# Kernel optimization log

Measured on AMD Instinct MI355X. Metric: run time of the kernel, lower is better.

The kernel has to match this reference:

```python
import jax, jax.numpy as jnp
import numpy as np

B, N, E = 2, 2048, 1024
H = 16
D = E // H  # head_dim = 64
MLP = 4096
EPS = 1e-5


def _layernorm(x, g, b):
    mu = jnp.mean(x, axis=-1, keepdims=True)
    var = jnp.var(x, axis=-1, keepdims=True)
    return (x - mu) * jax.lax.rsqrt(var + EPS) * g + b


def setup_inputs() -> dict:
    key = jax.random.key(0)
    ks = jax.random.split(key, 12)
    s_e = 1.0 / np.sqrt(E)
    s_m = 1.0 / np.sqrt(MLP)
    return {
        "x": jax.random.normal(ks[0], (B, N, E), jnp.float32),
        "w_qkv": jax.random.uniform(ks[1], (E, 3 * E), jnp.float32, -s_e, s_e),
        "b_qkv": jax.random.uniform(ks[2], (3 * E,), jnp.float32, -s_e, s_e),
        "w_proj": jax.random.uniform(ks[3], (E, E), jnp.float32, -s_e, s_e),
        "b_proj": jax.random.uniform(ks[4], (E,), jnp.float32, -s_e, s_e),
        "g1": jnp.ones((E,), jnp.float32),
        "beta1": jnp.zeros((E,), jnp.float32),
        "g2": jnp.ones((E,), jnp.float32),
        "beta2": jnp.zeros((E,), jnp.float32),
        "w_fc1": jax.random.uniform(ks[5], (E, MLP), jnp.float32, -s_e, s_e),
        "b_fc1": jax.random.uniform(ks[6], (MLP,), jnp.float32, -s_e, s_e),
        "w_fc2": jax.random.uniform(ks[7], (MLP, E), jnp.float32, -s_m, s_m),
        "b_fc2": jax.random.uniform(ks[8], (E,), jnp.float32, -s_m, s_m),
    }


def reference(x, w_qkv, b_qkv, w_proj, b_proj, g1, beta1, g2, beta2,
              w_fc1, b_fc1, w_fc2, b_fc2):
    scale = D ** (-0.5)
    # --- attention block (pre-norm) ---
    h = _layernorm(x, g1, beta1)
    qkv = (h @ w_qkv + b_qkv).reshape(B, N, 3, H, D)
    q, k, v = (qkv[:, :, i].transpose(0, 2, 1, 3) for i in range(3))  # [B,H,N,D]
    scores = jnp.einsum("bhnd,bhmd->bhnm", q, k) * scale  # [B,H,N,N]
    attn = jax.nn.softmax(scores, axis=-1)
    out = jnp.einsum("bhnm,bhmd->bhnd", attn, v)
    out = out.transpose(0, 2, 1, 3).reshape(B, N, E)
    x = x + (out @ w_proj + b_proj)
    # --- MLP block (pre-norm, exact GELU as in torch default) ---
    h = _layernorm(x, g2, beta2)
    h = jax.nn.gelu(h @ w_fc1 + b_fc1, approximate=False) @ w_fc2 + b_fc2
    return x + h
```

## Files before the change

kernel.cpp:

```cpp
#include <hip/hip_runtime.h>
#include <hip/hip_bf16.h>
#include <cmath>


typedef __hip_bfloat16 bf16;
typedef __bf16 bf16x8 __attribute__((ext_vector_type(8)));
typedef __bf16 bf16x4v __attribute__((ext_vector_type(4)));
typedef float  f32x4  __attribute__((ext_vector_type(4)));

#define CB 2
#define CN 2048
#define CE 1024
#define CH 16
#define CD 64
#define CMLP 4096
#define CM (CB*CN)

#define PS 136

#if __has_builtin(__builtin_amdgcn_exp2f)
#define EXP2F __builtin_amdgcn_exp2f
#else
#define EXP2F exp2f
#endif
#define SM_SCALE_LOG2E 0.18033688011112042f

__device__ __forceinline__ float b2f(bf16 v){ return __bfloat162float(v); }
__device__ __forceinline__ bf16  f2b(float v){ return __float2bfloat16(v); }

__device__ __forceinline__ void gl_lds16(const void* g, void* l){
  __builtin_amdgcn_global_load_lds((__attribute__((address_space(1))) void*)g,
                                   (__attribute__((address_space(3))) void*)l,
                                   16, 0, 0);
}

__global__ __launch_bounds__(256) void transpose_k(const float* __restrict__ in,
                                                   bf16* __restrict__ out,
                                                   int K, int N){
  __shared__ float tile[32][33];
  const int n0 = blockIdx.x*32, k0 = blockIdx.y*32;
  const int tx = threadIdx.x & 31;
  const int ty = threadIdx.x >> 5;
  #pragma unroll
  for(int i=0;i<32;i+=8) tile[ty+i][tx] = in[(size_t)(k0+ty+i)*N + n0+tx];
  __syncthreads();
  #pragma unroll
  for(int i=0;i<32;i+=8) out[(size_t)(n0+ty+i)*K + k0+tx] = f2b(tile[tx][ty+i]);
}

__global__ __launch_bounds__(256) void ln_k(const float* __restrict__ x,
                                            const float* __restrict__ g,
                                            const float* __restrict__ be,
                                            bf16* __restrict__ out){
  const int row = blockIdx.x;
  const int t = threadIdx.x;
  const float4 v4 = ((const float4*)(x + (size_t)row*CE))[t];
  float v[4] = {v4.x, v4.y, v4.z, v4.w};
  float s=0.f, s2=0.f;
  #pragma unroll
  for(int i=0;i<4;i++){ s+=v[i]; s2+=v[i]*v[i]; }
  #pragma unroll
  for(int off=32; off>0; off>>=1){ s += __shfl_down(s,off); s2 += __shfl_down(s2,off); }
  __shared__ float red[8];
  __shared__ float mu_s, rs_s;
  const int wv=t>>6, ln=t&63;
  if(ln==0){ red[wv]=s; red[4+wv]=s2; }
  __syncthreads();
  if(t==0){
    float S=red[0]+red[1]+red[2]+red[3], S2=red[4]+red[5]+red[6]+red[7];
    float mu=S/CE;
    mu_s=mu; rs_s=rsqrtf(S2/CE - mu*mu + 1e-5f);
  }
  __syncthreads();
  const float mu=mu_s, rs=rs_s;
  #pragma unroll
  for(int i=0;i<4;i++){
    int c=t*4+i;
    out[(size_t)row*CE+c] = f2b((v[i]-mu)*rs*g[c] + be[c]);
  }
}

#define EP_QKV 0
#define EP_GELU 2

template<int MODE>
__global__ __launch_bounds__(512,2) void gemm256_k(
  const bf16* __restrict__ A, const bf16* __restrict__ BT,
  const float* __restrict__ bias,
  bf16* __restrict__ Cb, bf16* __restrict__ Cq, bf16* __restrict__ Ck,
  bf16* __restrict__ Cv, int Ksz, int Nsz)
{
  __shared__ __align__(16) bf16 Alds[2][256*64];
  __shared__ __align__(16) bf16 Blds[2][256*64];
  const int tid = threadIdx.x;
  const int wave = tid>>6, lane = tid&63;
  const int m16 = lane&15, quad = lane>>4;
  const int sw = m16&7;
  const int wi = wave>>2, wj = wave&3;

  const int lin = blockIdx.x + gridDim.x*blockIdx.y;
  const int m_idx = (lin&7) + 8*((lin>>3)&1);
  const int n_idx = lin>>4;
  const size_t m0 = (size_t)m_idx*256;
  const size_t n0 = (size_t)n_idx*256;

  f32x4 acc[8][4] = {};

  const int srow8 = lane>>3;
  const int schk  = ((lane&7)^srow8)*8;
  const bf16* pA = A  + (m0 + 32*wave + srow8)*(size_t)Ksz + schk;
  const bf16* pB = BT + (n0 + 32*wave + srow8)*(size_t)Ksz + schk;

  auto stage = [&](int buf, const bf16* gA, const bf16* gB){
    bf16* lA = &Alds[buf][wave*2048];
    bf16* lB = &Blds[buf][wave*2048];
    #pragma unroll
    for(int j=0;j<4;j++) gl_lds16(gA + (size_t)(j*8)*Ksz, lA + j*512);
    #pragma unroll
    for(int j=0;j<4;j++) gl_lds16(gB + (size_t)(j*8)*Ksz, lB + j*512);
  };
  auto compute = [&](int buf){
    #pragma unroll
    for(int w=0;w<2;w++){
      bf16x8 af[8], bfr[4];
      #pragma unroll
      for(int i=0;i<8;i++){
        const int row = wi*128+16*i+m16;
        af[i] = *(const bf16x8*)(&Alds[buf][row*64 + ((w*4+quad)^sw)*8]);
      }
      #pragma unroll
      for(int j=0;j<4;j++){
        const int row = wj*64+16*j+m16;
        bfr[j] = *(const bf16x8*)(&Blds[buf][row*64 + ((w*4+quad)^sw)*8]);
      }
      #pragma unroll
      for(int i=0;i<8;i++)
        #pragma unroll
        for(int j=0;j<4;j++)
          acc[i][j] = __builtin_amdgcn_mfma_f32_16x16x32_bf16(af[i], bfr[j], acc[i][j], 0,0,0);
    }
  };

  const int kIters = Ksz/64;
  stage(0, pA, pB); pA += 64; pB += 64;
  for(int kb=0; kb<kIters; ++kb){
    __syncthreads();
    if(kb+1<kIters){ stage((kb+1)&1, pA, pB); pA += 64; pB += 64; }
    compute(kb&1);
  }

  #pragma unroll
  for(int i=0;i<8;i++){
    #pragma unroll
    for(int j=0;j<4;j++){
      const int col = (int)n0 + wj*64 + 16*j + m16;
      const float bcol = bias[col];
      #pragma unroll
      for(int r=0;r<4;r++){
        const int row = (int)m0 + wi*128 + 16*i + quad*4 + r;
        float v = acc[i][j][r] + bcol;
        if constexpr (MODE==EP_QKV){
          const int b = row>>11, n = row&2047;
          const int which = col>>10, cc = col&1023;
          const int h = cc>>6, d = cc&63;
          if(which==0)      Cq[(((size_t)(b*CH+h))*CN+n)*CD + d] = f2b(v);
          else if(which==1) Ck[(((size_t)(b*CH+h))*CN+n)*CD + d] = f2b(v);
          else              Cv[(((size_t)(b*CH+h))*CD+d)*CN + n] = f2b(v);
        } else {
          const float u2 = 1.5957691216f*(v + 0.044715f*v*v*v);
          v = v * (1.f/(1.f + __expf(-u2)));
          Cb[(size_t)row*Nsz+col] = f2b(v);
        }
      }
    }
  }
}

__global__ __launch_bounds__(512,2) void gemm128_k(
  const bf16* __restrict__ A, const bf16* __restrict__ BT,
  const float* __restrict__ bias, const float* __restrict__ res,
  float* __restrict__ Cf, int Ksz, int Nsz)
{
  __shared__ __align__(16) bf16 Alds[2][128*128];
  __shared__ __align__(16) bf16 Blds[2][128*128];
  const int tid = threadIdx.x;
  const int wave = tid>>6, lane = tid&63;
  const int m16 = lane&15, quad = lane>>4;
  const int sw = m16&7;
  const int wi = wave>>2, wj = wave&3;

  const int lin = blockIdx.x + gridDim.x*blockIdx.y;
  const int m_idx = (lin&7) + 8*((lin>>3)&3);
  const int n_idx = lin>>5;
  const size_t m0 = (size_t)m_idx*128;
  const size_t n0 = (size_t)n_idx*128;

  f32x4 acc[4][2] = {};

  const int rl = lane>>4;
  const int slot = lane&15;
  const int sce = (slot&8) | ((slot^rl)&7);
  const bf16* pAe = A  + (m0 + 16*wave + rl)*(size_t)Ksz + sce*8;
  const bf16* pAo = A  + (m0 + 16*wave + rl)*(size_t)Ksz + (sce^4)*8;
  const bf16* pBe = BT + (n0 + 16*wave + rl)*(size_t)Ksz + sce*8;
  const bf16* pBo = BT + (n0 + 16*wave + rl)*(size_t)Ksz + (sce^4)*8;

  auto stage = [&](int buf, size_t koff){
    bf16* lA = &Alds[buf][wave*16*128];
    bf16* lB = &Blds[buf][wave*16*128];
    #pragma unroll
    for(int j=0;j<4;j++){
      const bf16* sA = ((j&1)?pAo:pAe) + koff + (size_t)(4*j)*Ksz;
      const bf16* sB = ((j&1)?pBo:pBe) + koff + (size_t)(4*j)*Ksz;
      gl_lds16(sA, lA + j*512);
      gl_lds16(sB, lB + j*512);
    }
  };
  auto compute = [&](int buf){
    #pragma unroll
    for(int w=0;w<4;w++){
      bf16x8 af[4], bfr[2];
      #pragma unroll
      for(int i=0;i<4;i++){
        const int row = wi*64+16*i+m16;
        af[i] = *(const bf16x8*)(&Alds[buf][row*128 + ((w*4+quad)^sw)*8]);
      }
      #pragma unroll
      for(int j=0;j<2;j++){
        const int row = wj*32+16*j+m16;
        bfr[j] = *(const bf16x8*)(&Blds[buf][row*128 + ((w*4+quad)^sw)*8]);
      }
      #pragma unroll
      for(int i=0;i<4;i++)
        #pragma unroll
        for(int j=0;j<2;j++)
          acc[i][j] = __builtin_amdgcn_mfma_f32_16x16x32_bf16(af[i], bfr[j], acc[i][j], 0,0,0);
    }
  };

  const int kIters = Ksz/128;
  size_t koff = 128;
  stage(0, 0);
  for(int kb=0; kb<kIters; ++kb){
    __syncthreads();
    if(kb+1<kIters){ stage((kb+1)&1, koff); koff += 128; }
    compute(kb&1);
  }

  #pragma unroll
  for(int i=0;i<4;i++){
    #pragma unroll
    for(int j=0;j<2;j++){
      const int col = (int)n0 + wj*32 + 16*j + m16;
      const float bcol = bias[col];
      #pragma unroll
      for(int r=0;r<4;r++){
        const int row = (int)m0 + wi*64 + 16*i + quad*4 + r;
        float v = acc[i][j][r] + bcol + res[(size_t)row*Nsz+col];
        Cf[(size_t)row*Nsz+col] = v;
      }
    }
  }
}

__global__ __launch_bounds__(256,2) void attn_k(
  const bf16* __restrict__ Q, const bf16* __restrict__ Kx,
  const bf16* __restrict__ Vt, bf16* __restrict__ O)
{
  const int lin = blockIdx.x + gridDim.x*blockIdx.y;
  const int bh = (lin&7) + 8*(lin>>7);
  const int qblk = (lin>>3)&15;
  const int b = bh>>4, h = bh&15;
  const int tid = threadIdx.x;
  const int wave = tid>>6, lane = tid&63;
  const int m16 = lane&15, quad = lane>>4;
  const int sw = m16&7;
  const int q0 = qblk*128 + wave*32;

  const bf16* Qb = Q  + (size_t)bh*CN*CD;
  const bf16* Kb = Kx + (size_t)bh*CN*CD;
  const bf16* Vb = Vt + (size_t)bh*CD*CN;

  bf16x8 qf[2][2];
  #pragma unroll
  for(int g=0;g<2;g++){
    const bf16* qp = Qb + (size_t)(q0+g*16+m16)*CD + quad*8;
    qf[g][0] = *(const bf16x8*)(qp);
    qf[g][1] = *(const bf16x8*)(qp + 32);
  }

  float li[2] = {0.f, 0.f};
  f32x4 oacc[2][4] = {};

  __shared__ __align__(16) bf16 Klds[128*64];
  __shared__ __align__(16) bf16 Vlds[64*128];
  __shared__ __align__(16) bf16 Plds[4][32*PS];
  bf16* Pw = &Plds[wave][0];

  const int krow = wave*32 + (lane>>3);
  const int kchk = (lane&7) ^ (lane>>3);
  const bf16* pK = Kb + (size_t)krow*CD + kchk*8;
  const int vrow = wave*16 + (lane>>4);
  const bf16* pV[4];
  #pragma unroll
  for(int j=0;j<4;j++){
    const int ck = (lane&15) ^ ((j*4 + (lane>>4)) & 7);
    pV[j] = Vb + (size_t)(vrow + j*4)*CN + ck*8;
  }
  bf16* lK = Klds + wave*2048;
  bf16* lV = Vlds + wave*2048;

  for(int kt=0; kt<CN; kt+=128){
    __syncthreads();
    #pragma unroll
    for(int j=0;j<4;j++){
      gl_lds16(pK + (size_t)j*8*CD, lK + j*512);
      gl_lds16(pV[j],               lV + j*512);
      pV[j] += 128;
    }
    pK += (size_t)128*CD;
    __syncthreads();

    f32x4 sf0[8], sf1[8];
    #pragma unroll
    for(int f=0;f<8;f++){
      const bf16* kb = Klds + (f*16+m16)*64;
      bf16x8 k0 = *(const bf16x8*)(kb + ((quad   ^ sw)*8));
      bf16x8 k1 = *(const bf16x8*)(kb + (((quad+4)^ sw)*8));
      f32x4 t0 = {}, t1 = {};
      t0 = __builtin_amdgcn_mfma_f32_16x16x32_bf16(k0, qf[0][0], t0, 0,0,0);
      t0 = __builtin_amdgcn_mfma_f32_16x16x32_bf16(k1, qf[0][1], t0, 0,0,0);
      t1 = __builtin_amdgcn_mfma_f32_16x16x32_bf16(k0, qf[1][0], t1, 0,0,0);
      t1 = __builtin_amdgcn_mfma_f32_16x16x32_bf16(k1, qf[1][1], t1, 0,0,0);
      sf0[f]=t0; sf1[f]=t1;
    }
    #pragma unroll
    for(int f=0;f<8;f++){
      bf16x4v p0, p1;
      #pragma unroll
      for(int r=0;r<4;r++){
        float e0 = EXP2F(sf0[f][r]*SM_SCALE_LOG2E); li[0]+=e0; p0[r]=(__bf16)e0;
        float e1 = EXP2F(sf1[f][r]*SM_SCALE_LOG2E); li[1]+=e1; p1[r]=(__bf16)e1;
      }
      *(bf16x4v*)(Pw + (size_t)m16*PS       + f*16 + quad*4) = p0;
      *(bf16x4v*)(Pw + (size_t)(16+m16)*PS  + f*16 + quad*4) = p1;
    }
    asm volatile("s_waitcnt lgkmcnt(0)" ::: "memory");
    #pragma unroll
    for(int c=0;c<4;c++){
      const bf16x8 ap0 = *(const bf16x8*)(Pw + (size_t)m16*PS      + c*32 + quad*8);
      const bf16x8 ap1 = *(const bf16x8*)(Pw + (size_t)(16+m16)*PS + c*32 + quad*8);
      #pragma unroll
      for(int dt=0;dt<4;dt++){
        const int d = dt*16+m16;
        bf16x8 bv = *(const bf16x8*)(Vlds + d*128 + (((c*4+quad) ^ sw)*8));
        oacc[0][dt] = __builtin_amdgcn_mfma_f32_16x16x32_bf16(ap0, bv, oacc[0][dt], 0,0,0);
        oacc[1][dt] = __builtin_amdgcn_mfma_f32_16x16x32_bf16(ap1, bv, oacc[1][dt], 0,0,0);
      }
    }
  }
  #pragma unroll
  for(int g=0;g<2;g++){
    li[g] += __shfl_xor(li[g], 16);
    li[g] += __shfl_xor(li[g], 32);
  }
  #pragma unroll
  for(int g=0;g<2;g++){
    float linv[4];
    #pragma unroll
    for(int r=0;r<4;r++) linv[r] = 1.f / __shfl(li[g], quad*4+r);
    #pragma unroll
    for(int dt=0;dt<4;dt++){
      #pragma unroll
      for(int r=0;r<4;r++){
        const int row = q0 + g*16 + quad*4 + r;
        O[((size_t)(b*CN+row))*CE + h*CD + dt*16 + m16] = f2b(oacc[g][dt][r]*linv[r]);
      }
    }
  }
}

extern "C" void kernel_launch(void* const* d_in, const int* in_sizes, int n_in,
                              void* d_out, int out_size, void* d_ws, size_t ws_size,
                              hipStream_t stream)
{
  (void)in_sizes; (void)n_in; (void)out_size; (void)ws_size;
  const float* x     = (const float*)d_in[0];
  const float* w_qkv = (const float*)d_in[1];
  const float* b_qkv = (const float*)d_in[2];
  const float* w_proj= (const float*)d_in[3];
  const float* b_proj= (const float*)d_in[4];
  const float* g1    = (const float*)d_in[5];
  const float* be1   = (const float*)d_in[6];
  const float* g2    = (const float*)d_in[7];
  const float* be2   = (const float*)d_in[8];
  const float* w_fc1 = (const float*)d_in[9];
  const float* b_fc1 = (const float*)d_in[10];
  const float* w_fc2 = (const float*)d_in[11];
  const float* b_fc2 = (const float*)d_in[12];
  float* out = (float*)d_out;

  char* ws = (char*)d_ws;
  size_t off = 0;
  auto alloc = [&](size_t bytes)->char*{
    char* p = ws + off;
    off += (bytes + 255) & ~(size_t)255;
    return p;
  };
  bf16* wqkvT = (bf16*)alloc((size_t)3072*1024*2);
  bf16* wprojT= (bf16*)alloc((size_t)1024*1024*2);
  bf16* wfc1T = (bf16*)alloc((size_t)4096*1024*2);
  bf16* wfc2T = (bf16*)alloc((size_t)1024*4096*2);
  bf16* h1    = (bf16*)alloc((size_t)CM*CE*2);
  bf16* q     = (bf16*)alloc((size_t)CM*CE*2);
  bf16* kk    = (bf16*)alloc((size_t)CM*CE*2);
  bf16* vT    = (bf16*)alloc((size_t)CM*CE*2);
  bf16* aO    = (bf16*)alloc((size_t)CM*CE*2);
  float* x2   = (float*)alloc((size_t)CM*CE*4);
  bf16* hmlp  = q;

  transpose_k<<<dim3(3072/32,1024/32),256,0,stream>>>(w_qkv, wqkvT, 1024,3072);
  transpose_k<<<dim3(1024/32,1024/32),256,0,stream>>>(w_proj, wprojT,1024,1024);
  transpose_k<<<dim3(4096/32,1024/32),256,0,stream>>>(w_fc1, wfc1T, 1024,4096);
  transpose_k<<<dim3(1024/32,4096/32),256,0,stream>>>(w_fc2, wfc2T, 4096,1024);

  ln_k<<<CM,256,0,stream>>>(x, g1, be1, h1);
  gemm256_k<EP_QKV><<<dim3(3072/256, CM/256),512,0,stream>>>(
      h1, wqkvT, b_qkv, nullptr, q, kk, vT, 1024, 3072);
  attn_k<<<dim3(CN/128, CB*CH),256,0,stream>>>(q, kk, vT, aO);
  gemm128_k<<<dim3(1024/128, CM/128),512,0,stream>>>(
      aO, wprojT, b_proj, x, x2, 1024, 1024);
  ln_k<<<CM,256,0,stream>>>(x2, g2, be2, h1);
  gemm256_k<EP_GELU><<<dim3(4096/256, CM/256),512,0,stream>>>(
      h1, wfc1T, b_fc1, hmlp, nullptr, nullptr, nullptr, 1024, 4096);
  gemm128_k<<<dim3(1024/128, CM/128),512,0,stream>>>(
      hmlp, wfc2T, b_fc2, x2, out, 4096, 1024);
}
```

Before: 366.8 us.

## Pipeline large GEMM with split-half LDS staging and retile small-N GEMMs

Rewrites the 256x256 GEMM so each K step is split into half-tiles for A and B. Global-to-LDS loads for later half-tiles are interleaved between MFMA phases, with explicit vmcnt waits, raw barriers and s_setprio around the math, so loads overlap compute. The 128x128 projection and fc2 GEMMs become 128x64 tiles with 256 threads and K-step 64, doubling the number of blocks. It also drops the amdgcn exp2f builtin in favour of plain exp2f, which the attention kernel may use. The cost is many more barriers per iteration and hand-tuned wait counts that must stay correct.

New measurement: 374.0 us. About the same (+2.0%).

```diff
diff --git a/kernel.cpp b/kernel.cpp
--- a/kernel.cpp
+++ b/kernel.cpp
@@ -18,11 +18,7 @@
 
 #define PS 136
 
-#if __has_builtin(__builtin_amdgcn_exp2f)
-#define EXP2F __builtin_amdgcn_exp2f
-#else
 #define EXP2F exp2f
-#endif
 #define SM_SCALE_LOG2E 0.18033688011112042f
 
 __device__ __forceinline__ float b2f(bf16 v){ return __bfloat162float(v); }
@@ -33,6 +29,11 @@
                                    (__attribute__((address_space(3))) void*)l,
                                    16, 0, 0);
 }
+
+#define FENCE asm volatile("" ::: "memory")
+#define BAR   do{ FENCE; __builtin_amdgcn_s_barrier(); FENCE; }while(0)
+#define VMW4  asm volatile("s_waitcnt vmcnt(4)" ::: "memory")
+#define VMW0  asm volatile("s_waitcnt vmcnt(0)" ::: "memory")
 
 __global__ __launch_bounds__(256) void transpose_k(const float* __restrict__ in,
                                                    bf16* __restrict__ out,
@@ -84,19 +85,21 @@
 #define EP_GELU 2
 
 template<int MODE>
-__global__ __launch_bounds__(512,2) void gemm256_k(
+__global__ __launch_bounds__(512,2) void gemm256p_k(
   const bf16* __restrict__ A, const bf16* __restrict__ BT,
   const float* __restrict__ bias,
   bf16* __restrict__ Cb, bf16* __restrict__ Cq, bf16* __restrict__ Ck,
   bf16* __restrict__ Cv, int Ksz, int Nsz)
 {
-  __shared__ __align__(16) bf16 Alds[2][256*64];
-  __shared__ __align__(16) bf16 Blds[2][256*64];
+  __shared__ __align__(16) bf16 Alds[2][2][128*64];
+  __shared__ __align__(16) bf16 Blds[2][2][128*64];
   const int tid = threadIdx.x;
   const int wave = tid>>6, lane = tid&63;
   const int m16 = lane&15, quad = lane>>4;
   const int sw = m16&7;
   const int wi = wave>>2, wj = wave&3;
+  const int bh = wj>>1;
+  const int blr = (wj&1)*64;
 
   const int lin = blockIdx.x + gridDim.x*blockIdx.y;
   const int m_idx = (lin&7) + 8*((lin>>3)&1);
@@ -108,46 +111,76 @@
 
   const int srow8 = lane>>3;
   const int schk  = ((lane&7)^srow8)*8;
-  const bf16* pA = A  + (m0 + 32*wave + srow8)*(size_t)Ksz + schk;
-  const bf16* pB = BT + (n0 + 32*wave + srow8)*(size_t)Ksz + schk;
-
-  auto stage = [&](int buf, const bf16* gA, const bf16* gB){
-    bf16* lA = &Alds[buf][wave*2048];
-    bf16* lB = &Blds[buf][wave*2048];
-    #pragma unroll
-    for(int j=0;j<4;j++) gl_lds16(gA + (size_t)(j*8)*Ksz, lA + j*512);
-    #pragma unroll
-    for(int j=0;j<4;j++) gl_lds16(gB + (size_t)(j*8)*Ksz, lB + j*512);
+  const bf16* gA = A  + (m0 + wave*8 + srow8)*(size_t)Ksz + schk;
+  const bf16* gB = BT + (n0 + wave*8 + srow8)*(size_t)Ksz + schk;
+  const int ldso = wave*512;
+
+  auto stageA = [&](int buf, int h, int t){
+    const bf16* g = gA + (size_t)(h*128)*Ksz + (size_t)t*64;
+    gl_lds16(g,                  &Alds[buf][h][ldso]);
+    gl_lds16(g + (size_t)64*Ksz, &Alds[buf][h][ldso + 4096]);
   };
-  auto compute = [&](int buf){
-    #pragma unroll
-    for(int w=0;w<2;w++){
-      bf16x8 af[8], bfr[4];
-      #pragma unroll
-      for(int i=0;i<8;i++){
-        const int row = wi*128+16*i+m16;
-        af[i] = *(const bf16x8*)(&Alds[buf][row*64 + ((w*4+quad)^sw)*8]);
-      }
-      #pragma unroll
-      for(int j=0;j<4;j++){
-        const int row = wj*64+16*j+m16;
-        bfr[j] = *(const bf16x8*)(&Blds[buf][row*64 + ((w*4+quad)^sw)*8]);
-      }
-      #pragma unroll
-      for(int i=0;i<8;i++)
-        #pragma unroll
-        for(int j=0;j<4;j++)
-          acc[i][j] = __builtin_amdgcn_mfma_f32_16x16x32_bf16(af[i], bfr[j], acc[i][j], 0,0,0);
-    }
+  auto stageB = [&](int buf, int h, int t){
+    const bf16* g = gB + (size_t)(h*128)*Ksz + (size_t)t*64;
+    gl_lds16(g,                  &Blds[buf][h][ldso]);
+    gl_lds16(g + (size_t)64*Ksz, &Blds[buf][h][ldso + 4096]);
   };
 
-  const int kIters = Ksz/64;
-  stage(0, pA, pB); pA += 64; pB += 64;
-  for(int kb=0; kb<kIters; ++kb){
-    __syncthreads();
-    if(kb+1<kIters){ stage((kb+1)&1, pA, pB); pA += 64; pB += 64; }
-    compute(kb&1);
-  }
+  const int ck0 = ((quad  )^sw)*8;
+  const int ck1 = ((quad+4)^sw)*8;
+  bf16x8 af[4][2];
+  bf16x8 bfv[4][2];
+
+#define RD_A(BUF,RH) do{ _Pragma("unroll") for(int i_=0;i_<4;i_++){ \
+    const bf16* p_ = &Alds[BUF][wi][((RH)*64+16*i_+m16)*64]; \
+    af[i_][0] = *(const bf16x8*)(p_+ck0); af[i_][1] = *(const bf16x8*)(p_+ck1);} }while(0)
+#define RD_B(BUF,CH) do{ _Pragma("unroll") for(int j_=0;j_<2;j_++){ \
+    const bf16* p_ = &Blds[BUF][bh][(blr+((CH)*2+j_)*16+m16)*64]; \
+    bfv[(CH)*2+j_][0] = *(const bf16x8*)(p_+ck0); \
+    bfv[(CH)*2+j_][1] = *(const bf16x8*)(p_+ck1);} }while(0)
+#define MM(RH,CH) do{ __builtin_amdgcn_s_setprio(1); \
+    _Pragma("unroll") for(int i_=0;i_<4;i_++) _Pragma("unroll") for(int j_=0;j_<2;j_++){ \
+      acc[(RH)*4+i_][(CH)*2+j_] = __builtin_amdgcn_mfma_f32_16x16x32_bf16( \
+          af[i_][0], bfv[(CH)*2+j_][0], acc[(RH)*4+i_][(CH)*2+j_],0,0,0); \
+      acc[(RH)*4+i_][(CH)*2+j_] = __builtin_amdgcn_mfma_f32_16x16x32_bf16( \
+          af[i_][1], bfv[(CH)*2+j_][1], acc[(RH)*4+i_][(CH)*2+j_],0,0,0);} \
+    __builtin_amdgcn_s_setprio(0); }while(0)
+
+  stageA(0,0,0); stageA(0,1,0); stageB(0,0,0); stageB(0,1,0);
+  stageB(1,0,1); stageB(1,1,1);
+  VMW4; BAR;
+
+  const int nIter = Ksz/128;
+  #pragma unroll 1
+  for(int u=0; u<nIter; ++u){
+    const int t1 = 2*u+1, t2 = 2*u+2, t3 = 2*u+3;
+    const bool more = (u+1<nIter);
+    RD_A(0,0); RD_B(0,0);
+    stageA(1,0,t1);
+    BAR; MM(0,0); BAR;
+    RD_B(0,1);
+    stageA(1,1,t1);
+    BAR; MM(0,1); BAR;
+    RD_A(0,1);
+    if(more) stageB(0,0,t2);
+    BAR; MM(1,0); BAR;
+    if(more){ stageB(0,1,t2); VMW4; } else { VMW0; }
+    BAR; MM(1,1); BAR;
+    RD_A(1,0); RD_B(1,0);
+    if(more) stageA(0,0,t2);
+    BAR; MM(0,0); BAR;
+    RD_B(1,1);
+    if(more) stageA(0,1,t2);
+    BAR; MM(0,1); BAR;
+    RD_A(1,1);
+    if(more) stageB(1,0,t3);
+    BAR; MM(1,0); BAR;
+    if(more){ stageB(1,1,t3); VMW4; }
+    BAR; MM(1,1); BAR;
+  }
+#undef RD_A
+#undef RD_B
+#undef MM
 
   #pragma unroll
   for(int i=0;i<8;i++){
@@ -176,59 +209,53 @@
   }
 }
 
-__global__ __launch_bounds__(512,2) void gemm128_k(
+__global__ __launch_bounds__(256,2) void gemm64_k(
   const bf16* __restrict__ A, const bf16* __restrict__ BT,
   const float* __restrict__ bias, const float* __restrict__ res,
   float* __restrict__ Cf, int Ksz, int Nsz)
 {
-  __shared__ __align__(16) bf16 Alds[2][128*128];
-  __shared__ __align__(16) bf16 Blds[2][128*128];
+  __shared__ __align__(16) bf16 Alds[2][128*64];
+  __shared__ __align__(16) bf16 Blds[2][64*64];
   const int tid = threadIdx.x;
   const int wave = tid>>6, lane = tid&63;
   const int m16 = lane&15, quad = lane>>4;
-  const int sw = m16&7;
-  const int wi = wave>>2, wj = wave&3;
+  const int wi = wave>>1, wj = wave&1;
 
   const int lin = blockIdx.x + gridDim.x*blockIdx.y;
   const int m_idx = (lin&7) + 8*((lin>>3)&3);
   const int n_idx = lin>>5;
   const size_t m0 = (size_t)m_idx*128;
-  const size_t n0 = (size_t)n_idx*128;
+  const size_t n0 = (size_t)n_idx*64;
 
   f32x4 acc[4][2] = {};
 
-  const int rl = lane>>4;
-  const int slot = lane&15;
-  const int sce = (slot&8) | ((slot^rl)&7);
-  const bf16* pAe = A  + (m0 + 16*wave + rl)*(size_t)Ksz + sce*8;
-  const bf16* pAo = A  + (m0 + 16*wave + rl)*(size_t)Ksz + (sce^4)*8;
-  const bf16* pBe = BT + (n0 + 16*wave + rl)*(size_t)Ksz + sce*8;
-  const bf16* pBo = BT + (n0 + 16*wave + rl)*(size_t)Ksz + (sce^4)*8;
-
-  auto stage = [&](int buf, size_t koff){
-    bf16* lA = &Alds[buf][wave*16*128];
-    bf16* lB = &Blds[buf][wave*16*128];
-    #pragma unroll
-    for(int j=0;j<4;j++){
-      const bf16* sA = ((j&1)?pAo:pAe) + koff + (size_t)(4*j)*Ksz;
-      const bf16* sB = ((j&1)?pBo:pBe) + koff + (size_t)(4*j)*Ksz;
-      gl_lds16(sA, lA + j*512);
-      gl_lds16(sB, lB + j*512);
-    }
+  const int srow8 = lane>>3;
+  const int schk  = ((lane&7)^srow8)*8;
+  const bf16* pA = A  + (m0 + 32*wave + srow8)*(size_t)Ksz + schk;
+  const bf16* pB = BT + (n0 + 16*wave + srow8)*(size_t)Ksz + schk;
+
+  auto stage = [&](int buf, const bf16* gA, const bf16* gB){
+    bf16* lA = &Alds[buf][wave*2048];
+    bf16* lB = &Blds[buf][wave*1024];
+    #pragma unroll
+    for(int j=0;j<4;j++) gl_lds16(gA + (size_t)(j*8)*Ksz, lA + j*512);
+    #pragma unroll
+    for(int j=0;j<2;j++) gl_lds16(gB + (size_t)(j*8)*Ksz, lB + j*512);
   };
   auto compute = [&](int buf){
     #pragma unroll
-    for(int w=0;w<4;w++){
+    for(int w=0;w<2;w++){
+      const int swl = (m16&7);
       bf16x8 af[4], bfr[2];
       #pragma unroll
       for(int i=0;i<4;i++){
         const int row = wi*64+16*i+m16;
-        af[i] = *(const bf16x8*)(&Alds[buf][row*128 + ((w*4+quad)^sw)*8]);
+        af[i] = *(const bf16x8*)(&Alds[buf][row*64 + ((w*4+quad)^swl)*8]);
       }
       #pragma unroll
       for(int j=0;j<2;j++){
         const int row = wj*32+16*j+m16;
-        bfr[j] = *(const bf16x8*)(&Blds[buf][row*128 + ((w*4+quad)^sw)*8]);
+        bfr[j] = *(const bf16x8*)(&Blds[buf][row*64 + ((w*4+quad)^swl)*8]);
       }
       #pragma unroll
       for(int i=0;i<4;i++)
@@ -238,12 +265,11 @@
     }
   };
 
-  const int kIters = Ksz/128;
-  size_t koff = 128;
-  stage(0, 0);
+  const int kIters = Ksz/64;
+  stage(0, pA, pB); pA += 64; pB += 64;
   for(int kb=0; kb<kIters; ++kb){
     __syncthreads();
-    if(kb+1<kIters){ stage((kb+1)&1, koff); koff += 128; }
+    if(kb+1<kIters){ stage((kb+1)&1, pA, pB); pA += 64; pB += 64; }
     compute(kb&1);
   }
 
@@ -425,14 +451,14 @@
   transpose_k<<<dim3(1024/32,4096/32),256,0,stream>>>(w_fc2, wfc2T, 4096,1024);
 
   ln_k<<<CM,256,0,stream>>>(x, g1, be1, h1);
-  gemm256_k<EP_QKV><<<dim3(3072/256, CM/256),512,0,stream>>>(
+  gemm256p_k<EP_QKV><<<dim3(3072/256, CM/256),512,0,stream>>>(
       h1, wqkvT, b_qkv, nullptr, q, kk, vT, 1024, 3072);
   attn_k<<<dim3(CN/128, CB*CH),256,0,stream>>>(q, kk, vT, aO);
-  gemm128_k<<<dim3(1024/128, CM/128),512,0,stream>>>(
+  gemm64_k<<<dim3(1024/64, CM/128),256,0,stream>>>(
       aO, wprojT, b_proj, x, x2, 1024, 1024);
   ln_k<<<CM,256,0,stream>>>(x2, g2, be2, h1);
-  gemm256_k<EP_GELU><<<dim3(4096/256, CM/256),512,0,stream>>>(
+  gemm256p_k<EP_GELU><<<dim3(4096/256, CM/256),512,0,stream>>>(
       h1, wfc1T, b_fc1, hmlp, nullptr, nullptr, nullptr, 1024, 4096);
-  gemm128_k<<<dim3(1024/128, CM/128),512,0,stream>>>(
+  gemm64_k<<<dim3(1024/64, CM/128),256,0,stream>>>(
       hmlp, wfc2T, b_fc2, x2, out, 4096, 1024);
 }
```

## Shrink GEMM tiles and add triple-buffered LDS pipeline with explicit vmcnt waits

Applied to the files above, without the earlier changes.

Both GEMM kernels switch to narrower N tiles (256x128 for QKV/FC1, 128x64 for proj/FC2) with BK=64. The K loop becomes a three-stage ring: two stages are prefetched ahead, and a raw s_waitcnt vmcnt plus barrier replaces __syncthreads. The aim is to raise CTA count to fill more CUs and to hide global-to-LDS latency better. The cost is lower per-tile data reuse, and the big kernel's occupancy hint drops to one block per CU. The attention exp2 builtin is also replaced with plain exp2f.

New measurement: 394.1 us. 7.4% more time.

```diff
diff --git a/kernel.cpp b/kernel.cpp
--- a/kernel.cpp
+++ b/kernel.cpp
@@ -18,11 +18,7 @@
 
 #define PS 136
 
-#if __has_builtin(__builtin_amdgcn_exp2f)
-#define EXP2F __builtin_amdgcn_exp2f
-#else
 #define EXP2F exp2f
-#endif
 #define SM_SCALE_LOG2E 0.18033688011112042f
 
 __device__ __forceinline__ float b2f(bf16 v){ return __bfloat162float(v); }
@@ -33,6 +29,11 @@
                                    (__attribute__((address_space(3))) void*)l,
                                    16, 0, 0);
 }
+
+#define FENCE asm volatile("" ::: "memory")
+#define BAR   do{ FENCE; __builtin_amdgcn_s_barrier(); FENCE; }while(0)
+#define VMW6  asm volatile("s_waitcnt vmcnt(6)" ::: "memory")
+#define VMW0  asm volatile("s_waitcnt vmcnt(0)" ::: "memory")
 
 __global__ __launch_bounds__(256) void transpose_k(const float* __restrict__ in,
                                                    bf16* __restrict__ out,
@@ -84,14 +85,14 @@
 #define EP_GELU 2
 
 template<int MODE>
-__global__ __launch_bounds__(512,2) void gemm256_k(
+__global__ __launch_bounds__(512,1) void gemm256n_k(
   const bf16* __restrict__ A, const bf16* __restrict__ BT,
   const float* __restrict__ bias,
   bf16* __restrict__ Cb, bf16* __restrict__ Cq, bf16* __restrict__ Ck,
   bf16* __restrict__ Cv, int Ksz, int Nsz)
 {
-  __shared__ __align__(16) bf16 Alds[2][256*64];
-  __shared__ __align__(16) bf16 Blds[2][256*64];
+  __shared__ __align__(16) bf16 Alds[3][256*64];
+  __shared__ __align__(16) bf16 Blds[3][128*64];
   const int tid = threadIdx.x;
   const int wave = tid>>6, lane = tid&63;
   const int m16 = lane&15, quad = lane>>4;
@@ -99,61 +100,62 @@
   const int wi = wave>>2, wj = wave&3;
 
   const int lin = blockIdx.x + gridDim.x*blockIdx.y;
-  const int m_idx = (lin&7) + 8*((lin>>3)&1);
+  const int m_idx = lin&15;
   const int n_idx = lin>>4;
   const size_t m0 = (size_t)m_idx*256;
-  const size_t n0 = (size_t)n_idx*256;
-
-  f32x4 acc[8][4] = {};
+  const size_t n0 = (size_t)n_idx*128;
+
+  f32x4 acc[8][2] = {};
 
   const int srow8 = lane>>3;
   const int schk  = ((lane&7)^srow8)*8;
   const bf16* pA = A  + (m0 + 32*wave + srow8)*(size_t)Ksz + schk;
-  const bf16* pB = BT + (n0 + 32*wave + srow8)*(size_t)Ksz + schk;
-
-  auto stage = [&](int buf, const bf16* gA, const bf16* gB){
+  const bf16* pB = BT + (n0 + 16*wave + srow8)*(size_t)Ksz + schk;
+
+  auto stage = [&](int buf, size_t ko){
     bf16* lA = &Alds[buf][wave*2048];
-    bf16* lB = &Blds[buf][wave*2048];
-    #pragma unroll
-    for(int j=0;j<4;j++) gl_lds16(gA + (size_t)(j*8)*Ksz, lA + j*512);
-    #pragma unroll
-    for(int j=0;j<4;j++) gl_lds16(gB + (size_t)(j*8)*Ksz, lB + j*512);
+    bf16* lB = &Blds[buf][wave*1024];
+    #pragma unroll
+    for(int j=0;j<4;j++) gl_lds16(pA + ko + (size_t)(j*8)*Ksz, lA + j*512);
+    #pragma unroll
+    for(int j=0;j<2;j++) gl_lds16(pB + ko + (size_t)(j*8)*Ksz, lB + j*512);
   };
   auto compute = [&](int buf){
     #pragma unroll
     for(int w=0;w<2;w++){
-      bf16x8 af[8], bfr[4];
-      #pragma unroll
-      for(int i=0;i<8;i++){
-        const int row = wi*128+16*i+m16;
-        af[i] = *(const bf16x8*)(&Alds[buf][row*64 + ((w*4+quad)^sw)*8]);
-      }
-      #pragma unroll
-      for(int j=0;j<4;j++){
-        const int row = wj*64+16*j+m16;
-        bfr[j] = *(const bf16x8*)(&Blds[buf][row*64 + ((w*4+quad)^sw)*8]);
-      }
+      bf16x8 af[8], bfr[2];
+      #pragma unroll
+      for(int i=0;i<8;i++)
+        af[i] = *(const bf16x8*)(&Alds[buf][(wi*128+16*i+m16)*64 + ((w*4+quad)^sw)*8]);
+      #pragma unroll
+      for(int j=0;j<2;j++)
+        bfr[j] = *(const bf16x8*)(&Blds[buf][(wj*32+16*j+m16)*64 + ((w*4+quad)^sw)*8]);
       #pragma unroll
       for(int i=0;i<8;i++)
         #pragma unroll
-        for(int j=0;j<4;j++)
+        for(int j=0;j<2;j++)
           acc[i][j] = __builtin_amdgcn_mfma_f32_16x16x32_bf16(af[i], bfr[j], acc[i][j], 0,0,0);
     }
   };
 
   const int kIters = Ksz/64;
-  stage(0, pA, pB); pA += 64; pB += 64;
+  stage(0, 0); stage(1, 64);
+  size_t ko = 128;
+  int bc = 0, bs = 2;
   for(int kb=0; kb<kIters; ++kb){
-    __syncthreads();
-    if(kb+1<kIters){ stage((kb+1)&1, pA, pB); pA += 64; pB += 64; }
-    compute(kb&1);
+    if(kb==kIters-1){ VMW0; } else { VMW6; }
+    BAR;
+    if(kb+2<kIters){ stage(bs, ko); ko += 64; }
+    compute(bc);
+    bc = (bc==2)?0:bc+1;
+    bs = (bs==2)?0:bs+1;
   }
 
   #pragma unroll
   for(int i=0;i<8;i++){
     #pragma unroll
-    for(int j=0;j<4;j++){
-      const int col = (int)n0 + wj*64 + 16*j + m16;
+    for(int j=0;j<2;j++){
+      const int col = (int)n0 + wj*32 + 16*j + m16;
       const float bcol = bias[col];
       #pragma unroll
       for(int r=0;r<4;r++){
@@ -176,59 +178,53 @@
   }
 }
 
-__global__ __launch_bounds__(512,2) void gemm128_k(
+__global__ __launch_bounds__(256,2) void gemm64_k(
   const bf16* __restrict__ A, const bf16* __restrict__ BT,
   const float* __restrict__ bias, const float* __restrict__ res,
   float* __restrict__ Cf, int Ksz, int Nsz)
 {
-  __shared__ __align__(16) bf16 Alds[2][128*128];
-  __shared__ __align__(16) bf16 Blds[2][128*128];
+  __shared__ __align__(16) bf16 Alds[3][128*64];
+  __shared__ __align__(16) bf16 Blds[3][64*64];
   const int tid = threadIdx.x;
   const int wave = tid>>6, lane = tid&63;
   const int m16 = lane&15, quad = lane>>4;
-  const int sw = m16&7;
-  const int wi = wave>>2, wj = wave&3;
+  const int wi = wave>>1, wj = wave&1;
 
   const int lin = blockIdx.x + gridDim.x*blockIdx.y;
-  const int m_idx = (lin&7) + 8*((lin>>3)&3);
-  const int n_idx = lin>>5;
+  const int n_idx = (lin&7)*2 + ((lin>>3)&1);
+  const int m_idx = lin>>4;
   const size_t m0 = (size_t)m_idx*128;
-  const size_t n0 = (size_t)n_idx*128;
+  const size_t n0 = (size_t)n_idx*64;
 
   f32x4 acc[4][2] = {};
 
-  const int rl = lane>>4;
-  const int slot = lane&15;
-  const int sce = (slot&8) | ((slot^rl)&7);
-  const bf16* pAe = A  + (m0 + 16*wave + rl)*(size_t)Ksz + sce*8;
-  const bf16* pAo = A  + (m0 + 16*wave + rl)*(size_t)Ksz + (sce^4)*8;
-  const bf16* pBe = BT + (n0 + 16*wave + rl)*(size_t)Ksz + sce*8;
-  const bf16* pBo = BT + (n0 + 16*wave + rl)*(size_t)Ksz + (sce^4)*8;
-
-  auto stage = [&](int buf, size_t koff){
-    bf16* lA = &Alds[buf][wave*16*128];
-    bf16* lB = &Blds[buf][wave*16*128];
-    #pragma unroll
-    for(int j=0;j<4;j++){
-      const bf16* sA = ((j&1)?pAo:pAe) + koff + (size_t)(4*j)*Ksz;
-      const bf16* sB = ((j&1)?pBo:pBe) + koff + (size_t)(4*j)*Ksz;
-      gl_lds16(sA, lA + j*512);
-      gl_lds16(sB, lB + j*512);
-    }
+  const int srow8 = lane>>3;
+  const int schk  = ((lane&7)^srow8)*8;
+  const bf16* pA = A  + (m0 + 32*wave + srow8)*(size_t)Ksz + schk;
+  const bf16* pB = BT + (n0 + 16*wave + srow8)*(size_t)Ksz + schk;
+
+  auto stage = [&](int buf, size_t ko){
+    bf16* lA = &Alds[buf][wave*2048];
+    bf16* lB = &Blds[buf][wave*1024];
+    #pragma unroll
+    for(int j=0;j<4;j++) gl_lds16(pA + ko + (size_t)(j*8)*Ksz, lA + j*512);
+    #pragma unroll
+    for(int j=0;j<2;j++) gl_lds16(pB + ko + (size_t)(j*8)*Ksz, lB + j*512);
   };
   auto compute = [&](int buf){
     #pragma unroll
-    for(int w=0;w<4;w++){
+    for(int w=0;w<2;w++){
+      const int swl = (m16&7);
       bf16x8 af[4], bfr[2];
       #pragma unroll
       for(int i=0;i<4;i++){
         const int row = wi*64+16*i+m16;
-        af[i] = *(const bf16x8*)(&Alds[buf][row*128 + ((w*4+quad)^sw)*8]);
+        af[i] = *(const bf16x8*)(&Alds[buf][row*64 + ((w*4+quad)^swl)*8]);
       }
       #pragma unroll
       for(int j=0;j<2;j++){
         const int row = wj*32+16*j+m16;
-        bfr[j] = *(const bf16x8*)(&Blds[buf][row*128 + ((w*4+quad)^sw)*8]);
+        bfr[j] = *(const bf16x8*)(&Blds[buf][row*64 + ((w*4+quad)^swl)*8]);
       }
       #pragma unroll
       for(int i=0;i<4;i++)
@@ -238,13 +234,17 @@
     }
   };
 
-  const int kIters = Ksz/128;
-  size_t koff = 128;
-  stage(0, 0);
+  const int kIters = Ksz/64;
+  stage(0, 0); stage(1, 64);
+  size_t ko = 128;
+  int bc = 0, bs = 2;
   for(int kb=0; kb<kIters; ++kb){
-    __syncthreads();
-    if(kb+1<kIters){ stage((kb+1)&1, koff); koff += 128; }
-    compute(kb&1);
+    if(kb==kIters-1){ VMW0; } else { VMW6; }
+    BAR;
+    if(kb+2<kIters){ stage(bs, ko); ko += 64; }
+    compute(bc);
+    bc = (bc==2)?0:bc+1;
+    bs = (bs==2)?0:bs+1;
   }
 
   #pragma unroll
@@ -425,14 +425,14 @@
   transpose_k<<<dim3(1024/32,4096/32),256,0,stream>>>(w_fc2, wfc2T, 4096,1024);
 
   ln_k<<<CM,256,0,stream>>>(x, g1, be1, h1);
-  gemm256_k<EP_QKV><<<dim3(3072/256, CM/256),512,0,stream>>>(
+  gemm256n_k<EP_QKV><<<dim3(16, 3072/128),512,0,stream>>>(
       h1, wqkvT, b_qkv, nullptr, q, kk, vT, 1024, 3072);
   attn_k<<<dim3(CN/128, CB*CH),256,0,stream>>>(q, kk, vT, aO);
-  gemm128_k<<<dim3(1024/128, CM/128),512,0,stream>>>(
+  gemm64_k<<<dim3(16, 32),256,0,stream>>>(
       aO, wprojT, b_proj, x, x2, 1024, 1024);
   ln_k<<<CM,256,0,stream>>>(x2, g2, be2, h1);
-  gemm256_k<EP_GELU><<<dim3(4096/256, CM/256),512,0,stream>>>(
+  gemm256n_k<EP_GELU><<<dim3(16, 4096/128),512,0,stream>>>(
       h1, wfc1T, b_fc1, hmlp, nullptr, nullptr, nullptr, 1024, 4096);
-  gemm128_k<<<dim3(1024/128, CM/128),512,0,stream>>>(
+  gemm64_k<<<dim3(16, 32),256,0,stream>>>(
       hmlp, wfc2T, b_fc2, x2, out, 4096, 1024);
 }
```
